# Kernel tuning notes

Hardware: AMD Instinct MI355X
Metric: run time of the kernel (lower is better)

Reference implementation:

```python
import jax, jax.numpy as jnp
import numpy as np

B, N, C = 8, 196, 512
NC, H = 10, 8
HD = C // H
SCALE = HD ** -0.5


def setup_inputs() -> dict:
    key = jax.random.key(0)
    ks = jax.random.split(key, 8)
    s = 1.0 / np.sqrt(C)
    return {
        "x": jax.random.normal(ks[0], (B, N, C), jnp.float32),
        "anchors": jax.random.normal(ks[1], (NC, N, C), jnp.float32),
        "weights": jax.random.uniform(ks[2], (B, H, NC), jnp.float32),
        "Wqk": jax.random.normal(ks[3], (C, C), jnp.float32) * s,
        "Wqk2": jax.random.normal(ks[4], (C, C), jnp.float32) * s,
        "Wv": jax.random.normal(ks[5], (C, C), jnp.float32) * s,
        "Wproj": jax.random.normal(ks[6], (C, C), jnp.float32) * s,
        "bproj": jax.random.normal(ks[7], (C,), jnp.float32) * 0.01,
    }


def _heads(t):
    # (..., N, C) -> (..., H, N, HD)
    shp = t.shape[:-2]
    return t.reshape(shp + (t.shape[-2], H, HD)).swapaxes(-3, -2)


def reference(x, anchors, weights, Wqk, Wqk2, Wv, Wproj, bproj):
    v = _heads(x @ Wv)                      # (B, H, N, HD)
    q = _heads(x @ Wqk)[:, None]            # (B, 1, H, N, HD)
    k = _heads(anchors @ Wqk)[None]         # (1, NC, H, N, HD)
    q2 = _heads(x @ Wqk2)[:, None]          # (B, 1, H, N, HD)
    k2 = _heads(anchors @ Wqk2)[None]       # (1, NC, H, N, HD)

    # ReLU-clipped double attention, both (B, NC, H, N, N)
    left_attn = jnp.maximum(-(q @ k.swapaxes(-2, -1)) * SCALE, 0.0)
    right_attn = jnp.maximum((k2 @ q2.swapaxes(-2, -1)) * SCALE, 0.0)

    attn = left_attn @ right_attn           # (B, NC, H, N, N)
    # per-head class-weighted combine: (B,H,NC) x (B,NC,H,N,N) -> (B,H,N,N)
    tmp = jnp.einsum('bhc,bchnm->bhnm', weights, attn)
    out = tmp @ v                           # (B, H, N, HD)
    # NOTE: original torch code reshapes (B,H,N,HD)->(B,N,C) WITHOUT a
    # transpose back; we replicate that exact flatten order.
    out = out.reshape(B, N, C)
    out = out @ Wproj + bproj
    return (out, left_attn)
```

## Files before the change

### kernel.cpp

```cpp
#include <hip/hip_runtime.h>

#define OFF_XB     0u
#define OFF_AB     1605632u
#define OFF_WQKT   3612672u
#define OFF_WQK2T  4136960u
#define OFF_WVT    4661248u
#define OFF_WPROJT 5185536u
#define OFF_XQ     5709824u
#define OFF_XQ2    7315456u
#define OFF_XV     8921088u
#define OFF_AQ     10526720u
#define OFF_AQ2    12533760u
#define OFF_RVT    14540800u
#define OFF_OUT1   35512320u
#define OFF_P      37117952u

typedef __attribute__((ext_vector_type(8))) short bf16x8;
typedef __attribute__((ext_vector_type(4))) float f32x4;
#define MFMA(a, b, c) __builtin_amdgcn_mfma_f32_16x16x32_bf16((a), (b), (c), 0, 0, 0)

__device__ __forceinline__ unsigned short f2bf(float x) {
  unsigned u = __builtin_bit_cast(unsigned, x);
  u += 0x7fffu + ((u >> 16) & 1u);
  return (unsigned short)(u >> 16);
}
__device__ __forceinline__ float bf2f(unsigned short s) {
  return __builtin_bit_cast(float, ((unsigned)s) << 16);
}

__device__ __forceinline__ void gl_lds16(const void* g, void* l) {
  __builtin_amdgcn_global_load_lds(
      (const __attribute__((address_space(1))) unsigned int*)g,
      (__attribute__((address_space(3))) unsigned int*)l, 16, 0, 0);
}

__device__ __forceinline__ void stage64(const unsigned short* g0, int stride,
                                        unsigned short (*T)[72], int tid, int nrows) {
  int wv = tid >> 6;
  char* base = (char*)&T[0][0];
#pragma unroll
  for (int i = 0; i < 2; i++) {
    int k = i * 256 + tid;
    int r = k / 9, c = k - r * 9;
    if (r < nrows)
      gl_lds16(g0 + (size_t)r * stride + (c << 3), base + (((i << 2) + wv) << 10));
  }
  if (tid < 64) {
    int k = 512 + tid;
    int r = k / 9, c = k - r * 9;
    if (r < nrows)
      gl_lds16(g0 + (size_t)r * stride + (c << 3), base + 8192);
  }
}

__device__ __forceinline__ void vload_T(uint4* va, uint4* vb, const unsigned short* __restrict__ g,
                                        int row0, int nrows, int col0, int tid) {
  int j0 = tid >> 3, d0 = (tid & 7) << 3;
  *va = make_uint4(0, 0, 0, 0);
  *vb = make_uint4(0, 0, 0, 0);
  if (j0 < nrows) *va = *(const uint4*)(g + (size_t)(row0 + j0) * 512 + col0 + d0);
  if (j0 + 32 < nrows) *vb = *(const uint4*)(g + (size_t)(row0 + j0 + 32) * 512 + col0 + d0);
}
__device__ __forceinline__ void vwrite_T(unsigned short T[64][72], uint4 va, uint4 vb, int tid) {
  int j0 = tid >> 3, d0 = (tid & 7) << 3;
  unsigned short s[8];
  *(uint4*)s = va;
#pragma unroll
  for (int u = 0; u < 8; u++) T[d0 + u][j0] = s[u];
  *(uint4*)s = vb;
#pragma unroll
  for (int u = 0; u < 8; u++) T[d0 + u][j0 + 32] = s[u];
}

__global__ __launch_bounds__(256) void pre_kernel(const float* __restrict__ x, const float* __restrict__ anchors,
                                                  const float* __restrict__ Wqk, const float* __restrict__ Wqk2,
                                                  const float* __restrict__ Wv, const float* __restrict__ Wproj,
                                                  char* __restrict__ ws) {
  int tid = threadIdx.x;
  if (blockIdx.x < 1764) {
    int base = blockIdx.x * 1024 + (tid << 2);
    float4 f = (base < 802816) ? *(const float4*)(x + base)
                               : *(const float4*)(anchors + (base - 802816));
    unsigned short s[4] = {f2bf(f.x), f2bf(f.y), f2bf(f.z), f2bf(f.w)};
    *(uint2*)((unsigned short*)(ws + OFF_XB) + base) = *(uint2*)s;
    return;
  }
  __shared__ __align__(16) unsigned short Ls[64][72];
  int idx = blockIdx.x - 1764;
  int wsel = idx >> 6, t = idx & 63;
  int k0 = (t >> 3) << 6, n0 = (t & 7) << 6;
  const float* W;
  unsigned short* WT;
  switch (wsel) {
    case 0:  W = Wqk;   WT = (unsigned short*)(ws + OFF_WQKT);   break;
    case 1:  W = Wqk2;  WT = (unsigned short*)(ws + OFF_WQK2T);  break;
    case 2:  W = Wv;    WT = (unsigned short*)(ws + OFF_WVT);    break;
    default: W = Wproj; WT = (unsigned short*)(ws + OFF_WPROJT); break;
  }
  {
    int r = tid >> 2, seg = (tid & 3) << 4;
    const float* p = W + (size_t)(k0 + r) * 512 + n0 + seg;
    float4 f0 = *(const float4*)p, f1 = *(const float4*)(p + 4);
    float4 f2 = *(const float4*)(p + 8), f3 = *(const float4*)(p + 12);
    unsigned short s[16] = {f2bf(f0.x), f2bf(f0.y), f2bf(f0.z), f2bf(f0.w),
                            f2bf(f1.x), f2bf(f1.y), f2bf(f1.z), f2bf(f1.w),
                            f2bf(f2.x), f2bf(f2.y), f2bf(f2.z), f2bf(f2.w),
                            f2bf(f3.x), f2bf(f3.y), f2bf(f3.z), f2bf(f3.w)};
    *(uint4*)&Ls[r][seg] = *(uint4*)s;
    *(uint4*)&Ls[r][seg + 8] = *(uint4*)(s + 8);
  }
  __syncthreads();
  {
    int r = tid >> 2, seg = (tid & 3) << 4;
    unsigned short s[16];
#pragma unroll
    for (int u = 0; u < 16; u++) s[u] = Ls[seg + u][r];
    unsigned short* dst = WT + (size_t)(n0 + r) * 512 + k0 + seg;
    *(uint4*)dst = *(uint4*)s;
    *(uint4*)(dst + 8) = *(uint4*)(s + 8);
  }
}

template <bool STORE_BF16>
__device__ __forceinline__ void gemm_bf16_body(const unsigned short* __restrict__ A,
                                               const unsigned short* __restrict__ WT,
                                               const float* __restrict__ bias, void* __restrict__ outp,
                                               int M, int row_blk, int col_blk) {
  __shared__ __align__(16) unsigned short As[64][72];
  __shared__ __align__(16) unsigned short Ws[64][72];
  int row0 = row_blk << 6;
  if (row0 >= M) return;
  int col0 = col_blk << 6;
  int tid = threadIdx.x;
  int w = tid >> 6, lm = tid & 15, lq = (tid >> 4) & 3;
  f32x4 acc[4] = {};
  for (int k0 = 0; k0 < 512; k0 += 64) {
    __syncthreads();
    stage64(A + (size_t)row0 * 512 + k0, 512, As, tid, 64);
    stage64(WT + (size_t)col0 * 512 + k0, 512, Ws, tid, 64);
    __syncthreads();
#pragma unroll
    for (int kk = 0; kk < 2; kk++) {
      bf16x8 bf = *(const bf16x8*)&Ws[(w << 4) + lm][(kk << 5) + (lq << 3)];
#pragma unroll
      for (int mi = 0; mi < 4; mi++) {
        bf16x8 af = *(const bf16x8*)&As[(mi << 4) + lm][(kk << 5) + (lq << 3)];
        acc[mi] = MFMA(af, bf, acc[mi]);
      }
    }
  }
  int ncol = col0 + (w << 4) + lm;
  float bv = bias ? bias[ncol] : 0.f;
#pragma unroll
  for (int mi = 0; mi < 4; mi++)
#pragma unroll
    for (int r2 = 0; r2 < 4; r2++) {
      int row = row0 + (mi << 4) + (lq << 2) + r2;
      if (row < M) {
        if (STORE_BF16)
          ((unsigned short*)outp)[(size_t)row * 512 + ncol] = f2bf(acc[mi][r2]);
        else
          ((float*)outp)[(size_t)row * 512 + ncol] = acc[mi][r2] + bv;
      }
    }
}

__global__ __launch_bounds__(256) void proj5(char* __restrict__ ws) {
  const unsigned short* xb = (const unsigned short*)(ws + OFF_XB);
  const unsigned short* ab = (const unsigned short*)(ws + OFF_AB);
  const unsigned short* A; const unsigned short* WT; unsigned short* O; int M;
  switch (blockIdx.z) {
    case 0:  A = xb; WT = (unsigned short*)(ws + OFF_WQKT);  O = (unsigned short*)(ws + OFF_XQ);  M = 1568; break;
    case 1:  A = xb; WT = (unsigned short*)(ws + OFF_WQK2T); O = (unsigned short*)(ws + OFF_XQ2); M = 1568; break;
    case 2:  A = xb; WT = (unsigned short*)(ws + OFF_WVT);   O = (unsigned short*)(ws + OFF_XV);  M = 1568; break;
    case 3:  A = ab; WT = (unsigned short*)(ws + OFF_WQKT);  O = (unsigned short*)(ws + OFF_AQ);  M = 1960; break;
    default: A = ab; WT = (unsigned short*)(ws + OFF_WQK2T); O = (unsigned short*)(ws + OFF_AQ2); M = 1960; break;
  }
  gemm_bf16_body<true>(A, WT, nullptr, O, M, blockIdx.x, blockIdx.y);
}

__global__ __launch_bounds__(256) void final_gemm(const unsigned short* __restrict__ out1,
                                                  const unsigned short* __restrict__ WT,
                                                  const float* __restrict__ bias, float* __restrict__ out) {
  gemm_bf16_body<false>(out1, WT, bias, out, 1568, blockIdx.x, blockIdx.y);
}

__global__ __launch_bounds__(256) void rv_mfma(char* __restrict__ ws) {
  const unsigned short* xq2 = (const unsigned short*)(ws + OFF_XQ2);
  const unsigned short* aq2 = (const unsigned short*)(ws + OFF_AQ2);
  const unsigned short* xv  = (const unsigned short*)(ws + OFF_XV);
  unsigned short* rvt       = (unsigned short*)(ws + OFF_RVT);
  __shared__ __align__(16) unsigned short Qs[64][72];
  __shared__ __align__(16) unsigned short Vt[64][72];
  __shared__ __align__(16) unsigned short Ss[64][72];
  int d = blockIdx.x;
  int wk = ((d & 7) * 320) + (d >> 3);
  int it = wk & 3;
  int g = wk >> 2;
  int bh = g / 10, c = g - bh * 10;
  int b = bh >> 3, h = bh & 7;
  int bch = (b * 10 + c) * 8 + h;
  int i0 = it << 6;
  int tid = threadIdx.x;
  int w = tid >> 6, lm = tid & 15, lq = (tid >> 4) & 3;
  int iglob = i0 + (w << 4) + lm;

  bf16x8 kb[2] = {};
  if (iglob < 196) {
    const unsigned short* kp = aq2 + (size_t)(c * 196 + iglob) * 512 + (h << 6) + (lq << 3);
    kb[0] = *(const bf16x8*)kp;
    kb[1] = *(const bf16x8*)(kp + 32);
  }
  stage64(xq2 + (size_t)(b * 196) * 512 + (h << 6), 512, Qs, tid, 64);
  uint4 va, vb;
  vload_T(&va, &vb, xv, b * 196, 64, h << 6, tid);

  f32x4 acc[4] = {};
#pragma unroll
  for (int jt = 0; jt < 4; jt++) {
    int j0 = jt << 6;
    __syncthreads();
    vwrite_T(Vt, va, vb, tid);
    f32x4 s[4] = {};
#pragma unroll
    for (int kk = 0; kk < 2; kk++)
#pragma unroll
      for (int mj = 0; mj < 4; mj++) {
        bf16x8 af = *(const bf16x8*)&Qs[(mj << 4) + lm][(kk << 5) + (lq << 3)];
        s[mj] = MFMA(af, kb[kk], s[mj]);
      }
#pragma unroll
    for (int mj = 0; mj < 4; mj++) {
      unsigned short u[4] = {f2bf(fmaxf(0.125f * s[mj][0], 0.f)), f2bf(fmaxf(0.125f * s[mj][1], 0.f)),
                             f2bf(fmaxf(0.125f * s[mj][2], 0.f)), f2bf(fmaxf(0.125f * s[mj][3], 0.f))};
      *(uint2*)&Ss[(w << 4) + lm][(mj << 4) + (lq << 2)] = *(uint2*)u;
    }
    if (jt < 3) vload_T(&va, &vb, xv, b * 196 + j0 + 64, min(64, 196 - j0 - 64), h << 6, tid);
    __syncthreads();
    if (jt < 3) stage64(xq2 + (size_t)(b * 196 + j0 + 64) * 512 + (h << 6), 512, Qs, tid, 64);
#pragma unroll
    for (int kk = 0; kk < 2; kk++) {
      bf16x8 bf = *(const bf16x8*)&Vt[(w << 4) + lm][(kk << 5) + (lq << 3)];
#pragma unroll
      for (int mi = 0; mi < 4; mi++) {
        bf16x8 af = *(const bf16x8*)&Ss[(mi << 4) + lm][(kk << 5) + (lq << 3)];
        acc[mi] = MFMA(af, bf, acc[mi]);
      }
    }
  }
  __syncthreads();
#pragma unroll
  for (int mi = 0; mi < 4; mi++) {
    unsigned short u[4] = {f2bf(acc[mi][0]), f2bf(acc[mi][1]), f2bf(acc[mi][2]), f2bf(acc[mi][3])};
    *(uint2*)&Ss[(w << 4) + lm][(mi << 4) + (lq << 2)] = *(uint2*)u;
  }
  __syncthreads();
  {
    int dd = tid >> 2, seg = (tid & 3) << 4;
    unsigned short* dst = rvt + ((size_t)(bch * 4 + it) * 64 + dd) * 64 + seg;
    *(uint4*)dst = *(uint4*)&Ss[dd][seg];
    *(uint4*)(dst + 8) = *(uint4*)&Ss[dd][seg + 8];
  }
}

__global__ __launch_bounds__(256) void attn_mfma(char* __restrict__ ws, float* __restrict__ left,
                                                 unsigned short* __restrict__ P) {
  const unsigned short* xq  = (const unsigned short*)(ws + OFF_XQ);
  const unsigned short* aq  = (const unsigned short*)(ws + OFF_AQ);
  const unsigned short* rvt = (const unsigned short*)(ws + OFF_RVT);
  __shared__ __align__(16) unsigned short Ks[64][72];
  __shared__ __align__(16) unsigned short Ss[64][72];
  int d = blockIdx.x;
  int wk = ((d & 7) * 320) + (d >> 3);
  int i0 = (wk & 3) << 6;
  int g = wk >> 2;
  int c = g >> 6;
  int bh = g & 63;
  int b = bh >> 3, h = bh & 7;
  int bch = (b * 10 + c) * 8 + h;
  int tid = threadIdx.x;
  int w = tid >> 6, lm = tid & 15, lq = (tid >> 4) & 3;
  int iglob = i0 + (w << 4) + lm;

  bf16x8 qb[2];
  {
    const unsigned short* qp = xq + (size_t)(b * 196 + iglob) * 512 + (h << 6) + (lq << 3);
    qb[0] = *(const bf16x8*)qp;
    qb[1] = *(const bf16x8*)(qp + 32);
  }
  {
    uint4 z = make_uint4(0, 0, 0, 0);
    for (int k = tid; k < 540; k += 256)
      *(uint4*)((char*)&Ks[0][0] + 576 + k * 16) = z;
  }
  stage64(aq + (size_t)(c * 196 + 192) * 512 + (h << 6), 512, Ks, tid, 4);
  const unsigned short* rbase = rvt + (size_t)bch * 16384 + (((w << 4) + lm) << 6) + (lq << 3);
  bf16x8 rv0 = *(const bf16x8*)(rbase + 3 * 4096);
  bf16x8 rv1 = *(const bf16x8*)(rbase + 3 * 4096 + 32);

  f32x4 acc[4] = {};
  size_t lbase = (size_t)bch * (196 * 196);
#pragma unroll
  for (int t = 0; t < 4; t++) {
    int jt = (t == 0) ? 3 : t - 1;
    int j0 = jt << 6;
    __syncthreads();
    f32x4 s[4] = {};
#pragma unroll
    for (int kk = 0; kk < 2; kk++)
#pragma unroll
      for (int mj = 0; mj < 4; mj++) {
        bf16x8 af = *(const bf16x8*)&Ks[(mj << 4) + lm][(kk << 5) + (lq << 3)];
        s[mj] = MFMA(af, qb[kk], s[mj]);
      }
#pragma unroll
    for (int mj = 0; mj < 4; mj++) {
      f32x4 lv;
      lv[0] = fmaxf(-0.125f * s[mj][0], 0.f);
      lv[1] = fmaxf(-0.125f * s[mj][1], 0.f);
      lv[2] = fmaxf(-0.125f * s[mj][2], 0.f);
      lv[3] = fmaxf(-0.125f * s[mj][3], 0.f);
      int jloc = (mj << 4) + (lq << 2);
      if (iglob < 196 && j0 + jloc < 196)
        *(f32x4*)&left[lbase + (size_t)iglob * 196 + j0 + jloc] = lv;
      unsigned short u[4] = {f2bf(lv[0]), f2bf(lv[1]), f2bf(lv[2]), f2bf(lv[3])};
      *(uint2*)&Ss[(w << 4) + lm][jloc] = *(uint2*)u;
    }
    __syncthreads();
    if (t < 3)
      stage64(aq + (size_t)(c * 196 + (t << 6)) * 512 + (h << 6), 512, Ks, tid, 64);
    bf16x8 cur0 = rv0, cur1 = rv1;
    if (t < 3) {
      rv0 = *(const bf16x8*)(rbase + t * 4096);
      rv1 = *(const bf16x8*)(rbase + t * 4096 + 32);
    }
#pragma unroll
    for (int kk = 0; kk < 2; kk++) {
      bf16x8 bf = (kk == 0) ? cur0 : cur1;
#pragma unroll
      for (int mi = 0; mi < 4; mi++) {
        bf16x8 af = *(const bf16x8*)&Ss[(mi << 4) + lm][(kk << 5) + (lq << 3)];
        acc[mi] = MFMA(af, bf, acc[mi]);
      }
    }
  }
  __syncthreads();
#pragma unroll
  for (int mi = 0; mi < 4; mi++)
#pragma unroll
    for (int r = 0; r < 4; r++)
      Ss[(mi << 4) + (lq << 2) + r][(w << 4) + lm] = f2bf(acc[mi][r]);
  __syncthreads();
  {
    int row = tid >> 2, seg = (tid & 3) << 4;
    if (i0 + row < 196) {
      unsigned short* dst = P + ((size_t)(bh * 10 + c) * 196 + i0 + row) * 64 + seg;
      *(uint4*)dst = *(uint4*)&Ss[row][seg];
      *(uint4*)(dst + 8) = *(uint4*)&Ss[row][seg + 8];
    }
  }
}

__global__ __launch_bounds__(256) void reduce_out1(const unsigned short* __restrict__ P,
                                                   const float* __restrict__ weights,
                                                   unsigned short* __restrict__ out1) {
  int t = blockIdx.x * 256 + threadIdx.x;
  int base = t << 2;
  int bh = base / 12544;
  int rem = base - bh * 12544;
  const float* wrow = weights + bh * 10;
  float a0 = 0.f, a1 = 0.f, a2 = 0.f, a3 = 0.f;
#pragma unroll
  for (int c = 0; c < 10; c++) {
    float wc = wrow[c];
    const unsigned short* p = P + ((size_t)(bh * 10 + c)) * 12544 + rem;
    ushort4 u = *(const ushort4*)p;
    a0 = fmaf(wc, bf2f(u.x), a0);
    a1 = fmaf(wc, bf2f(u.y), a1);
    a2 = fmaf(wc, bf2f(u.z), a2);
    a3 = fmaf(wc, bf2f(u.w), a3);
  }
  unsigned short s[4] = {f2bf(a0), f2bf(a1), f2bf(a2), f2bf(a3)};
  *(uint2*)&out1[base] = *(uint2*)s;
}

extern "C" void kernel_launch(void* const* d_in, const int* in_sizes, int n_in,
                              void* d_out, int out_size, void* d_ws, size_t ws_size,
                              hipStream_t stream) {
  (void)in_sizes; (void)n_in; (void)out_size; (void)ws_size;
  const float* x       = (const float*)d_in[0];
  const float* anchors = (const float*)d_in[1];
  const float* weights = (const float*)d_in[2];
  const float* Wqk     = (const float*)d_in[3];
  const float* Wqk2    = (const float*)d_in[4];
  const float* Wv      = (const float*)d_in[5];
  const float* Wproj   = (const float*)d_in[6];
  const float* bproj   = (const float*)d_in[7];
  char* ws = (char*)d_ws;
  float* out  = (float*)d_out;
  float* left = out + 802816;

  dim3 blk(256);
  pre_kernel<<<dim3(2020), blk, 0, stream>>>(x, anchors, Wqk, Wqk2, Wv, Wproj, ws);
  proj5<<<dim3(31, 8, 5), blk, 0, stream>>>(ws);
  rv_mfma<<<dim3(2560), blk, 0, stream>>>(ws);
  attn_mfma<<<dim3(2560), blk, 0, stream>>>(ws, left, (unsigned short*)(ws + OFF_P));
  reduce_out1<<<dim3(784), blk, 0, stream>>>((const unsigned short*)(ws + OFF_P), weights,
                                             (unsigned short*)(ws + OFF_OUT1));
  final_gemm<<<dim3(25, 8), blk, 0, stream>>>((const unsigned short*)(ws + OFF_OUT1),
                                              (const unsigned short*)(ws + OFF_WPROJT), bproj, out);
}
```

Measured before the change: 217.0 us.

## Share input tiles across projections and fold class reduction into attention

The five projection GEMM launches become one kernel. Each block stages an x or anchor tile once and multiplies it against two or three weight tiles, which cuts repeated A-tile loads but uses more shared memory and more accumulator registers per block. The separate reduce_out1 kernel is removed. Each attention block now increments a per-(bh, tile) atomic counter, and the last of the ten class blocks does the weighted class sum into out1. The counters live in the WQK2T weight region, reused as scratch and zeroed by rv_mfma. This saves a launch and a full pass over P, at the cost of a serialized tail reduction in the finishing block.

```diff
diff --git a/kernel.cpp b/kernel.cpp
--- a/kernel.cpp
+++ b/kernel.cpp
@@ -14,6 +14,7 @@
 #define OFF_RVT    14540800u
 #define OFF_OUT1   35512320u
 #define OFF_P      37117952u
+#define OFF_CNT    OFF_WQK2T
 
 typedef __attribute__((ext_vector_type(8))) short bf16x8;
 typedef __attribute__((ext_vector_type(4))) float f32x4;
@@ -121,22 +122,86 @@
   }
 }
 
-template <bool STORE_BF16>
-__device__ __forceinline__ void gemm_bf16_body(const unsigned short* __restrict__ A,
-                                               const unsigned short* __restrict__ WT,
-                                               const float* __restrict__ bias, void* __restrict__ outp,
-                                               int M, int row_blk, int col_blk) {
+template <int NW>
+__device__ __forceinline__ void proj_body(const unsigned short* __restrict__ A,
+                                          const unsigned short* W0, const unsigned short* W1,
+                                          const unsigned short* W2,
+                                          unsigned short* O0, unsigned short* O1, unsigned short* O2,
+                                          int M, unsigned short (*As)[72], unsigned short (*Wsh)[72]) {
+  int row0 = (int)blockIdx.x << 6;
+  if (row0 >= M) return;
+  int col0 = (int)blockIdx.y << 6;
+  int tid = threadIdx.x;
+  int w = tid >> 6, lm = tid & 15, lq = (tid >> 4) & 3;
+  const unsigned short* WTs[3] = {W0, W1, W2};
+  unsigned short* Os[3] = {O0, O1, O2};
+  f32x4 acc[NW][4] = {};
+  for (int k0 = 0; k0 < 512; k0 += 64) {
+    __syncthreads();
+    stage64(A + (size_t)row0 * 512 + k0, 512, As, tid, 64);
+#pragma unroll
+    for (int ww = 0; ww < NW; ww++)
+      stage64(WTs[ww] + (size_t)col0 * 512 + k0, 512,
+              (unsigned short(*)[72])&Wsh[ww << 6], tid, 64);
+    __syncthreads();
+#pragma unroll
+    for (int kk = 0; kk < 2; kk++) {
+      bf16x8 af[4];
+#pragma unroll
+      for (int mi = 0; mi < 4; mi++)
+        af[mi] = *(const bf16x8*)&As[(mi << 4) + lm][(kk << 5) + (lq << 3)];
+#pragma unroll
+      for (int ww = 0; ww < NW; ww++) {
+        bf16x8 bf = *(const bf16x8*)&Wsh[(ww << 6) + (w << 4) + lm][(kk << 5) + (lq << 3)];
+#pragma unroll
+        for (int mi = 0; mi < 4; mi++) acc[ww][mi] = MFMA(af[mi], bf, acc[ww][mi]);
+      }
+    }
+  }
+  int ncol = col0 + (w << 4) + lm;
+#pragma unroll
+  for (int ww = 0; ww < NW; ww++)
+#pragma unroll
+    for (int mi = 0; mi < 4; mi++)
+#pragma unroll
+      for (int r2 = 0; r2 < 4; r2++) {
+        int row = row0 + (mi << 4) + (lq << 2) + r2;
+        if (row < M)
+          Os[ww][(size_t)row * 512 + ncol] = f2bf(acc[ww][mi][r2]);
+      }
+}
+
+__global__ __launch_bounds__(256) void proj_combo(char* __restrict__ ws) {
+  __shared__ __align__(16) unsigned short As[64][72];
+  __shared__ __align__(16) unsigned short Wsh[192][72];
+  const unsigned short* xb = (const unsigned short*)(ws + OFF_XB);
+  const unsigned short* ab = (const unsigned short*)(ws + OFF_AB);
+  const unsigned short* wqkt  = (const unsigned short*)(ws + OFF_WQKT);
+  const unsigned short* wqk2t = (const unsigned short*)(ws + OFF_WQK2T);
+  const unsigned short* wvt   = (const unsigned short*)(ws + OFF_WVT);
+  if (blockIdx.z == 0)
+    proj_body<3>(xb, wqkt, wqk2t, wvt,
+                 (unsigned short*)(ws + OFF_XQ), (unsigned short*)(ws + OFF_XQ2),
+                 (unsigned short*)(ws + OFF_XV), 1568, As, Wsh);
+  else
+    proj_body<2>(ab, wqkt, wqk2t, nullptr,
+                 (unsigned short*)(ws + OFF_AQ), (unsigned short*)(ws + OFF_AQ2),
+                 nullptr, 1960, As, Wsh);
+}
+
+__global__ __launch_bounds__(256) void final_gemm(const unsigned short* __restrict__ out1,
+                                                  const unsigned short* __restrict__ WT,
+                                                  const float* __restrict__ bias, float* __restrict__ out) {
   __shared__ __align__(16) unsigned short As[64][72];
   __shared__ __align__(16) unsigned short Ws[64][72];
-  int row0 = row_blk << 6;
-  if (row0 >= M) return;
-  int col0 = col_blk << 6;
+  int row0 = (int)blockIdx.x << 6;
+  int col0 = (int)blockIdx.y << 6;
   int tid = threadIdx.x;
   int w = tid >> 6, lm = tid & 15, lq = (tid >> 4) & 3;
   f32x4 acc[4] = {};
   for (int k0 = 0; k0 < 512; k0 += 64) {
     __syncthreads();
-    stage64(A + (size_t)row0 * 512 + k0, 512, As, tid, 64);
+    stage64(out1 + (size_t)row0 * 512 + k0, 512, As, tid, 64);
     stage64(WT + (size_t)col0 * 512 + k0, 512, Ws, tid, 64);
     __syncthreads();
 #pragma unroll
@@ -150,39 +215,15 @@
     }
   }
   int ncol = col0 + (w << 4) + lm;
-  float bv = bias ? bias[ncol] : 0.f;
+  float bv = bias[ncol];
 #pragma unroll
   for (int mi = 0; mi < 4; mi++)
 #pragma unroll
     for (int r2 = 0; r2 < 4; r2++) {
       int row = row0 + (mi << 4) + (lq << 2) + r2;
-      if (row < M) {
-        if (STORE_BF16)
-          ((unsigned short*)outp)[(size_t)row * 512 + ncol] = f2bf(acc[mi][r2]);
-        else
-          ((float*)outp)[(size_t)row * 512 + ncol] = acc[mi][r2] + bv;
-      }
-    }
-}
-
-__global__ __launch_bounds__(256) void proj5(char* __restrict__ ws) {
-  const unsigned short* xb = (const unsigned short*)(ws + OFF_XB);
-  const unsigned short* ab = (const unsigned short*)(ws + OFF_AB);
-  const unsigned short* A; const unsigned short* WT; unsigned short* O; int M;
-  switch (blockIdx.z) {
-    case 0:  A = xb; WT = (unsigned short*)(ws + OFF_WQKT);  O = (unsigned short*)(ws + OFF_XQ);  M = 1568; break;
-    case 1:  A = xb; WT = (unsigned short*)(ws + OFF_WQK2T); O = (unsigned short*)(ws + OFF_XQ2); M = 1568; break;
-    case 2:  A = xb; WT = (unsigned short*)(ws + OFF_WVT);   O = (unsigned short*)(ws + OFF_XV);  M = 1568; break;
-    case 3:  A = ab; WT = (unsigned short*)(ws + OFF_WQKT);  O = (unsigned short*)(ws + OFF_AQ);  M = 1960; break;
-    default: A = ab; WT = (unsigned short*)(ws + OFF_WQK2T); O = (unsigned short*)(ws + OFF_AQ2); M = 1960; break;
-  }
-  gemm_bf16_body<true>(A, WT, nullptr, O, M, blockIdx.x, blockIdx.y);
-}
-
-__global__ __launch_bounds__(256) void final_gemm(const unsigned short* __restrict__ out1,
-                                                  const unsigned short* __restrict__ WT,
-                                                  const float* __restrict__ bias, float* __restrict__ out) {
-  gemm_bf16_body<false>(out1, WT, bias, out, 1568, blockIdx.x, blockIdx.y);
+      if (row < 1568)
+        out[(size_t)row * 512 + ncol] = acc[mi][r2] + bv;
+    }
 }
 
 __global__ __launch_bounds__(256) void rv_mfma(char* __restrict__ ws) {
@@ -193,6 +234,8 @@
   __shared__ __align__(16) unsigned short Qs[64][72];
   __shared__ __align__(16) unsigned short Vt[64][72];
   __shared__ __align__(16) unsigned short Ss[64][72];
+  int tid = threadIdx.x;
+  if (blockIdx.x == 0) ((unsigned*)(ws + OFF_CNT))[tid] = 0;
   int d = blockIdx.x;
   int wk = ((d & 7) * 320) + (d >> 3);
   int it = wk & 3;
@@ -201,7 +244,6 @@
   int b = bh >> 3, h = bh & 7;
   int bch = (b * 10 + c) * 8 + h;
   int i0 = it << 6;
-  int tid = threadIdx.x;
   int w = tid >> 6, lm = tid & 15, lq = (tid >> 4) & 3;
   int iglob = i0 + (w << 4) + lm;
 
@@ -264,15 +306,20 @@
 }
 
 __global__ __launch_bounds__(256) void attn_mfma(char* __restrict__ ws, float* __restrict__ left,
-                                                 unsigned short* __restrict__ P) {
+                                                 unsigned short* __restrict__ P,
+                                                 const float* __restrict__ weights) {
   const unsigned short* xq  = (const unsigned short*)(ws + OFF_XQ);
   const unsigned short* aq  = (const unsigned short*)(ws + OFF_AQ);
   const unsigned short* rvt = (const unsigned short*)(ws + OFF_RVT);
+  unsigned* cnt             = (unsigned*)(ws + OFF_CNT);
+  unsigned short* out1      = (unsigned short*)(ws + OFF_OUT1);
   __shared__ __align__(16) unsigned short Ks[64][72];
   __shared__ __align__(16) unsigned short Ss[64][72];
+  __shared__ unsigned oldc_s;
   int d = blockIdx.x;
   int wk = ((d & 7) * 320) + (d >> 3);
-  int i0 = (wk & 3) << 6;
+  int it = wk & 3;
+  int i0 = it << 6;
   int g = wk >> 2;
   int c = g >> 6;
   int bh = g & 63;
@@ -359,29 +406,34 @@
       *(uint4*)(dst + 8) = *(uint4*)&Ss[row][seg + 8];
     }
   }
-}
-
-__global__ __launch_bounds__(256) void reduce_out1(const unsigned short* __restrict__ P,
-                                                   const float* __restrict__ weights,
-                                                   unsigned short* __restrict__ out1) {
-  int t = blockIdx.x * 256 + threadIdx.x;
-  int base = t << 2;
-  int bh = base / 12544;
-  int rem = base - bh * 12544;
-  const float* wrow = weights + bh * 10;
-  float a0 = 0.f, a1 = 0.f, a2 = 0.f, a3 = 0.f;
-#pragma unroll
-  for (int c = 0; c < 10; c++) {
-    float wc = wrow[c];
-    const unsigned short* p = P + ((size_t)(bh * 10 + c)) * 12544 + rem;
-    ushort4 u = *(const ushort4*)p;
-    a0 = fmaf(wc, bf2f(u.x), a0);
-    a1 = fmaf(wc, bf2f(u.y), a1);
-    a2 = fmaf(wc, bf2f(u.z), a2);
-    a3 = fmaf(wc, bf2f(u.w), a3);
-  }
-  unsigned short s[4] = {f2bf(a0), f2bf(a1), f2bf(a2), f2bf(a3)};
-  *(uint2*)&out1[base] = *(uint2*)s;
+  __threadfence();
+  __syncthreads();
+  if (tid == 0) oldc_s = atomicAdd(&cnt[(bh << 2) + it], 1u);
+  __syncthreads();
+  if (oldc_s == 9) {
+    __threadfence();
+    const float* wrow = weights + bh * 10;
+#pragma unroll
+    for (int e = 0; e < 4; e++) {
+      int idx = ((e << 8) + tid) << 2;
+      int row = idx >> 6, dd = idx & 63;
+      if (i0 + row < 196) {
+        float a0 = 0.f, a1 = 0.f, a2 = 0.f, a3 = 0.f;
+#pragma unroll
+        for (int c2 = 0; c2 < 10; c2++) {
+          float wc = wrow[c2];
+          const unsigned short* p = P + ((size_t)(bh * 10 + c2) * 196 + i0 + row) * 64 + dd;
+          ushort4 u = *(const ushort4*)p;
+          a0 = fmaf(wc, bf2f(u.x), a0);
+          a1 = fmaf(wc, bf2f(u.y), a1);
+          a2 = fmaf(wc, bf2f(u.z), a2);
+          a3 = fmaf(wc, bf2f(u.w), a3);
+        }
+        unsigned short sb[4] = {f2bf(a0), f2bf(a1), f2bf(a2), f2bf(a3)};
+        *(uint2*)&out1[(size_t)bh * 12544 + (size_t)(i0 + row) * 64 + dd] = *(uint2*)sb;
+      }
+    }
+  }
 }
 
 extern "C" void kernel_launch(void* const* d_in, const int* in_sizes, int n_in,
@@ -402,11 +454,9 @@
 
   dim3 blk(256);
   pre_kernel<<<dim3(2020), blk, 0, stream>>>(x, anchors, Wqk, Wqk2, Wv, Wproj, ws);
-  proj5<<<dim3(31, 8, 5), blk, 0, stream>>>(ws);
+  proj_combo<<<dim3(31, 8, 2), blk, 0, stream>>>(ws);
   rv_mfma<<<dim3(2560), blk, 0, stream>>>(ws);
-  attn_mfma<<<dim3(2560), blk, 0, stream>>>(ws, left, (unsigned short*)(ws + OFF_P));
-  reduce_out1<<<dim3(784), blk, 0, stream>>>((const unsigned short*)(ws + OFF_P), weights,
-                                             (unsigned short*)(ws + OFF_OUT1));
+  attn_mfma<<<dim3(2560), blk, 0, stream>>>(ws, left, (unsigned short*)(ws + OFF_P), weights);
   final_gemm<<<dim3(25, 8), blk, 0, stream>>>((const unsigned short*)(ws + OFF_OUT1),
                                               (const unsigned short*)(ws + OFF_WPROJT), bproj, out);
 }
```

Measured after the change: 744.9 us. 243% more time.
